# Kernel optimization log

Measured on AMD Instinct MI355X. Metric: run time of the kernel, lower is better.

## Reference

```python
import jax, jax.numpy as jnp
from jax import lax
import numpy as np

B, T, D_IN, H, L, D_OUT = 1024, 512, 6, 128, 3, 1


def _lstm_layer(xs, w_ih, w_hh, b_ih, b_hh):
    """xs: [B, T, Din]; w_ih: [4H, Din]; w_hh: [4H, H]. PyTorch gate order i,f,g,o."""
    Bq = xs.shape[0]
    Hq = w_hh.shape[1]
    # Precompute the input projection for all timesteps (compute-dense part).
    x_proj = jnp.einsum('btd,gd->btg', xs, w_ih) + (b_ih + b_hh)  # [B, T, 4H]

    def step(carry, xp):
        h, c = carry
        gates = xp + h @ w_hh.T  # [B, 4H]
        i, f, g, o = jnp.split(gates, 4, axis=-1)
        i = jax.nn.sigmoid(i)
        f = jax.nn.sigmoid(f)
        g = jnp.tanh(g)
        o = jax.nn.sigmoid(o)
        c = f * c + i * g
        h = o * jnp.tanh(c)
        return (h, c), h

    h0 = jnp.zeros((Bq, Hq), xs.dtype)
    c0 = jnp.zeros((Bq, Hq), xs.dtype)
    (_, _), hs = lax.scan(step, (h0, c0), jnp.swapaxes(x_proj, 0, 1))  # hs: [T, B, H]
    return jnp.swapaxes(hs, 0, 1)  # [B, T, H]


def setup_inputs() -> dict:
    key = jax.random.key(0)
    ks = jax.random.split(key, 16)
    s = 1.0 / np.sqrt(H)  # PyTorch LSTM init scale
    inp = {"x": jax.random.normal(ks[0], (B, T, D_IN), dtype=jnp.float32)}
    din = D_IN
    for l in range(L):
        inp[f"w_ih{l}"] = jax.random.uniform(ks[1 + 4 * l], (4 * H, din), minval=-s, maxval=s, dtype=jnp.float32)
        inp[f"w_hh{l}"] = jax.random.uniform(ks[2 + 4 * l], (4 * H, H), minval=-s, maxval=s, dtype=jnp.float32)
        inp[f"b_ih{l}"] = jax.random.uniform(ks[3 + 4 * l], (4 * H,), minval=-s, maxval=s, dtype=jnp.float32)
        inp[f"b_hh{l}"] = jax.random.uniform(ks[4 + 4 * l], (4 * H,), minval=-s, maxval=s, dtype=jnp.float32)
        din = H
    inp["fc_w"] = jax.random.uniform(ks[13], (D_OUT, H), minval=-s, maxval=s, dtype=jnp.float32)
    inp["fc_b"] = jax.random.uniform(ks[14], (D_OUT,), minval=-s, maxval=s, dtype=jnp.float32)
    return inp


def reference(x, w_ih0, w_hh0, b_ih0, b_hh0, w_ih1, w_hh1, b_ih1, b_hh1,
              w_ih2, w_hh2, b_ih2, b_hh2, fc_w, fc_b):
    # 3-layer LSTM (inference: dropout between layers is identity) + final Linear on last timestep.
    h = _lstm_layer(x, w_ih0, w_hh0, b_ih0, b_hh0)
    h = _lstm_layer(h, w_ih1, w_hh1, b_ih1, b_hh1)
    h = _lstm_layer(h, w_ih2, w_hh2, b_ih2, b_hh2)
    return h[:, -1, :] @ fc_w.T + fc_b  # [B, 1]
```

## Files before the change

kernel.cpp:

```cpp
#include <hip/hip_runtime.h>

#define TLEN  512
#define HID   128
#define RSLOT 16

typedef __attribute__((ext_vector_type(8))) short          bf16x8;
typedef __attribute__((ext_vector_type(4))) float          f32x4;
typedef __attribute__((ext_vector_type(2))) float          f32x2;
typedef __attribute__((ext_vector_type(4))) unsigned short u16x4;
typedef unsigned long long u64;

#define LOG2E  1.4426950408889634f
#define LOG2E2 2.8853900817779268f

template<bool B> struct BC { static constexpr bool value = B; };
template<int I>  struct IC { static constexpr int  value = I; };

__device__ __forceinline__ unsigned short f2bf(float f) {
    union { float f; unsigned u; } v; v.f = f;
    unsigned r = v.u + 0x7fffu + ((v.u >> 16) & 1u);
    return (unsigned short)(r >> 16);
}
__device__ __forceinline__ unsigned short f2bf_fast(float f) {
    union { float f; unsigned u; } v; v.f = f;
    return (unsigned short)((v.u + 0x8000u) >> 16);
}

__device__ __forceinline__ f32x2 exp2_2(f32x2 a) {
    f32x2 r; r.x = __builtin_exp2f(a.x); r.y = __builtin_exp2f(a.y); return r;
}
__device__ __forceinline__ f32x2 rcp_2(f32x2 a) {
    f32x2 r; r.x = __builtin_amdgcn_rcpf(a.x); r.y = __builtin_amdgcn_rcpf(a.y); return r;
}


__device__ __forceinline__ int flag_peek(const int* f) {
    return __hip_atomic_load(f, __ATOMIC_RELAXED, __HIP_MEMORY_SCOPE_AGENT);
}
__device__ __forceinline__ int flag_spin(const int* f, int v) {
    int x = flag_peek(f);
    while (x < v) { __builtin_amdgcn_s_sleep(1); x = flag_peek(f); }
    return x;
}
__device__ __forceinline__ void flag_pub(int* f, int v) {
    __hip_atomic_store(f, v, __ATOMIC_RELAXED, __HIP_MEMORY_SCOPE_WORKGROUP);
}

template<int MODE, bool CONS, bool PROD, bool WFC>
__device__ __forceinline__ void run_layer_p(
    const float* __restrict__ xin,
    const u64* __restrict__ rin, u64* __restrict__ rout,
    const int* pin_flag, int* cout_flag, const int* cin_flag, int* pout_flag,
    const float* __restrict__ wih, const float* __restrict__ whh,
    const float* __restrict__ bih, const float* __restrict__ bhh,
    unsigned short (* __restrict__ hbuf)[2048],
    unsigned short (* __restrict__ xbuf)[2048],
    float* __restrict__ fcred,
    const int tid, const int wave, const int lane,
    const int n16, const int quad, const int bbase)
{
    constexpr int NKTX = MODE ? 4 : 1;
    constexpr int DINL = MODE ? 128 : 6;

    bf16x8 Wfx[4][NKTX], Wfh[4][4];
    f32x4  bbv[4];
#pragma unroll
    for (int g = 0; g < 4; ++g) {
        const float sc = (g == 2) ? LOG2E2 : LOG2E;
        const int row = g * 128 + wave * 16 + n16;
        const float bg = (bih[row] + bhh[row]) * sc;
        f32x4 bi = {bg, bg, bg, bg};
        bbv[g] = bi;
#pragma unroll
        for (int kt = 0; kt < NKTX; ++kt) {
            bf16x8 wv;
#pragma unroll
            for (int j = 0; j < 8; ++j) {
                const int k = kt * 32 + quad * 8 + j;
                wv[j] = (short)f2bf(((k < DINL) ? wih[row * DINL + k] : 0.0f) * sc);
            }
            Wfx[g][kt] = wv;
        }
#pragma unroll
        for (int kt = 0; kt < 4; ++kt) {
            bf16x8 wv;
#pragma unroll
            for (int j = 0; j < 8; ++j) {
                const int k = kt * 32 + quad * 8 + j;
                wv[j] = (short)f2bf(whh[row * HID + k] * sc);
            }
            Wfh[g][kt] = wv;
        }
    }

    const int rof  = (lane ^ quad) * 8;
    const int j    = wave * 16 + n16;
    const int beta = ((j & 31) >> 3) & 3;
    const int wbase = ((j >> 5) * 64 + ((j & 31) >> 3) * 16 + quad * 4) * 8 + (j & 7);
    int wof[4];
#pragma unroll
    for (int r = 0; r < 4; ++r) wof[r] = wbase + ((r ^ beta) * 8);
    const int uof  = ((((tid >> 1) ^ ((tid >> 5) & 3))) << 3) + (tid & 1) * 4;
    const int xm = tid >> 5, xk = tid & 31;
    const int eiS = ((xk >> 3) * 16 + (xm ^ (xk >> 3))) * 8 + (xk & 7);

    { u16x4 z = {0, 0, 0, 0}; *(u16x4*)&hbuf[0][uof] = z; }
    u64 q0 = 0, q1 = 0, q2 = 0, qn = 0;
    float pfx0 = 0.0f;
    int pend = 0, cpend = 0;
    if constexpr (CONS) {
        flag_spin(pin_flag, 1);
        *(u64*)&xbuf[0][uof] =
            __hip_atomic_load(rin + tid, __ATOMIC_RELAXED, __HIP_MEMORY_SCOPE_AGENT);
        flag_spin(pin_flag, 2);
        *(u64*)&xbuf[1][uof] =
            __hip_atomic_load(rin + 512 + tid, __ATOMIC_RELAXED, __HIP_MEMORY_SCOPE_AGENT);
        pend = flag_spin(pin_flag, 5);
        q0 = __hip_atomic_load(rin + 2 * 512 + tid, __ATOMIC_RELAXED, __HIP_MEMORY_SCOPE_AGENT);
        q1 = __hip_atomic_load(rin + 3 * 512 + tid, __ATOMIC_RELAXED, __HIP_MEMORY_SCOPE_AGENT);
        q2 = __hip_atomic_load(rin + 4 * 512 + tid, __ATOMIC_RELAXED, __HIP_MEMORY_SCOPE_AGENT);
    } else {
        float v0 = (xk < DINL) ? xin[((bbase + xm) * TLEN + 0) * DINL + xk] : 0.0f;
        float v1 = (xk < DINL) ? xin[((bbase + xm) * TLEN + 1) * DINL + xk] : 0.0f;
        xbuf[0][eiS] = f2bf(v0);
        xbuf[1][eiS] = f2bf(v1);
        if (xk < DINL) pfx0 = xin[((bbase + xm) * TLEN + 2) * DINL + xk];
    }
    if constexpr (PROD) cpend = -(1 << 30);
    __syncthreads();

    f32x4 accA[4], accB[4];
#pragma unroll
    for (int kt = 0; kt < NKTX; ++kt) {
        bf16x8 a = *(const bf16x8*)&xbuf[0][rof + kt * 512];
#pragma unroll
        for (int g = 0; g < 4; ++g)
            accA[g] = __builtin_amdgcn_mfma_f32_16x16x32_bf16(
                a, Wfx[g][kt], (kt == 0) ? bbv[g] : accA[g], 0, 0, 0);
    }

    f32x2 cst2[2] = {{0.f, 0.f}, {0.f, 0.f}};
    float hf[4];

    auto step = [&](auto SHc, auto CMc, auto CURc, auto RDc, auto WRc,
                    f32x4 (&accC)[4], f32x4 (&accN)[4], int t) {
        constexpr bool SH  = decltype(SHc)::value;
        constexpr bool CM  = decltype(CMc)::value;
        constexpr int  CUR = decltype(CURc)::value;
        constexpr int  NXT = CUR ^ 1;
        constexpr int  RD  = decltype(RDc)::value;
        constexpr int  WR  = decltype(WRc)::value;
        __syncthreads();

        const unsigned short* __restrict__ hcur = hbuf[CUR];
        const unsigned short* __restrict__ xrd  = xbuf[RD];

        bf16x8 ha_[4], xa_[NKTX];
#pragma unroll
        for (int kt = 0; kt < 4; ++kt) ha_[kt] = *(const bf16x8*)&hcur[rof + kt * 512];
        if constexpr (SH) {
#pragma unroll
            for (int kt = 0; kt < NKTX; ++kt)
                xa_[kt] = *(const bf16x8*)&xrd[rof + kt * 512];
        }

        if constexpr (CONS) {
            if (t + 5 < TLEN) {
                if (pend < t + 6) pend = flag_spin(pin_flag, t + 6);
                qn = __hip_atomic_load(rin + ((t + 5) & (RSLOT - 1)) * 512 + tid,
                                       __ATOMIC_RELAXED, __HIP_MEMORY_SCOPE_AGENT);
                pend = flag_peek(pin_flag);
            }
        }
        if (tid == 0) {
            if constexpr (CONS) if ((t & 3) == 0) flag_pub(cout_flag, t + 5);
            if constexpr (PROD) if (t >= 2)       flag_pub(pout_flag, t - 1);
        }
        if constexpr (PROD) {
            if (t >= 1) {
                const int e = t - 1;
                if ((e & 3) == 0 && e + 4 > RSLOT && cpend < e + 4 - RSLOT)
                    cpend = flag_spin(cin_flag, e + 4 - RSLOT);
                u64 hv = *(const u64*)&hcur[uof];
                __hip_atomic_store(rout + (e & (RSLOT - 1)) * 512 + tid, hv,
                                   __ATOMIC_RELAXED, __HIP_MEMORY_SCOPE_WORKGROUP);
                if ((e & 3) == 1) cpend = flag_peek(cin_flag);
            }
        }
        float pfx1 = 0.0f;
        if constexpr (!CONS) {
            if (t + 3 < TLEN && xk < DINL)
                pfx1 = xin[((bbase + xm) * TLEN + (t + 3)) * DINL + xk];
        }

#pragma unroll
        for (int kt = 0; kt < 4; ++kt)
#pragma unroll
            for (int g = 0; g < 4; ++g)
                accC[g] = __builtin_amdgcn_mfma_f32_16x16x32_bf16(ha_[kt], Wfh[g][kt], accC[g], 0, 0, 0);

        if constexpr (SH) {
#pragma unroll
            for (int kt = 0; kt < NKTX; ++kt)
#pragma unroll
                for (int g = 0; g < 4; ++g)
                    accN[g] = __builtin_amdgcn_mfma_f32_16x16x32_bf16(
                        xa_[kt], Wfx[g][kt], (kt == 0) ? bbv[g] : accN[g], 0, 0, 0);
        }

        const f32x2 one = {1.0f, 1.0f};
#pragma unroll
        for (int p = 0; p < 2; ++p) {
            const f32x2 gi = {accC[0][2 * p], accC[0][2 * p + 1]};
            const f32x2 gf = {accC[1][2 * p], accC[1][2 * p + 1]};
            const f32x2 gg = {accC[2][2 * p], accC[2][2 * p + 1]};
            const f32x2 go = {accC[3][2 * p], accC[3][2 * p + 1]};
            const f32x2 A  = exp2_2(-gi);
            const f32x2 Fv = rcp_2(one + exp2_2(-gf));
            const f32x2 E  = exp2_2(-gg);
            const f32x2 D  = exp2_2(-go);
            const f32x2 ig = (one - E) * rcp_2((one + A) * (one + E));
            const f32x2 c  = Fv * cst2[p] + ig;
            cst2[p] = c;
            f32x2 y = c * (f32x2){LOG2E2, LOG2E2};
            y.x = fminf(fmaxf(y.x, -30.0f), 30.0f);
            y.y = fminf(fmaxf(y.y, -30.0f), 30.0f);
            const f32x2 Cn = exp2_2(-y);
            const f32x2 h2 = (one - Cn) * rcp_2((one + D) * (one + Cn));
            if constexpr (WFC) { hf[2 * p] = h2.x; hf[2 * p + 1] = h2.y; }
            hbuf[NXT][wof[2 * p]]     = f2bf_fast(h2.x);
            hbuf[NXT][wof[2 * p + 1]] = f2bf_fast(h2.y);
        }
        if constexpr (WFC) {
            if (t == TLEN - 1)
#pragma unroll
                for (int r = 0; r < 4; ++r)
                    fcred[(quad * 4 + r) * HID + wave * 16 + n16] = hf[r];
        }
        if constexpr (CM) {
            if constexpr (CONS) {
                *(u64*)&xbuf[WR][uof] = q0;
                q0 = q1; q1 = q2; q2 = qn;
            } else {
                xbuf[WR][eiS] = f2bf(pfx0);
                pfx0 = pfx1;
            }
        }
    };

    for (int t = 0; t < TLEN - 2; t += 6) {
        step(BC<true>{}, BC<true>{}, IC<0>{}, IC<1>{}, IC<2>{}, accA, accB, t);
        step(BC<true>{}, BC<true>{}, IC<1>{}, IC<2>{}, IC<0>{}, accB, accA, t + 1);
        step(BC<true>{}, BC<true>{}, IC<0>{}, IC<0>{}, IC<1>{}, accA, accB, t + 2);
        step(BC<true>{}, BC<true>{}, IC<1>{}, IC<1>{}, IC<2>{}, accB, accA, t + 3);
        step(BC<true>{}, BC<true>{}, IC<0>{}, IC<2>{}, IC<0>{}, accA, accB, t + 4);
        step(BC<true>{}, BC<true>{}, IC<1>{}, IC<0>{}, IC<1>{}, accB, accA, t + 5);
    }
    step(BC<true>{},  BC<false>{}, IC<0>{}, IC<1>{}, IC<2>{}, accA, accB, TLEN - 2);
    step(BC<false>{}, BC<false>{}, IC<1>{}, IC<2>{}, IC<0>{}, accB, accA, TLEN - 1);

    if constexpr (PROD) {
        __syncthreads();
        if (tid == 0) flag_pub(pout_flag, TLEN - 1);
        {
            flag_spin(cin_flag, TLEN - RSLOT);
            u64 hv = *(const u64*)&hbuf[TLEN & 1][uof];
            __hip_atomic_store(rout + ((TLEN - 1) & (RSLOT - 1)) * 512 + tid, hv,
                               __ATOMIC_RELAXED, __HIP_MEMORY_SCOPE_WORKGROUP);
        }
        __syncthreads();
        if (tid == 0) flag_pub(pout_flag, TLEN);
    }
}

extern "C" __global__ __launch_bounds__(512, 1)
void lstm3_pipe_kernel(const float* __restrict__ xin,
    const float* __restrict__ wih0, const float* __restrict__ whh0,
    const float* __restrict__ bih0, const float* __restrict__ bhh0,
    const float* __restrict__ wih1, const float* __restrict__ whh1,
    const float* __restrict__ bih1, const float* __restrict__ bhh1,
    const float* __restrict__ wih2, const float* __restrict__ whh2,
    const float* __restrict__ bih2, const float* __restrict__ bhh2,
    const float* __restrict__ fcw, const float* __restrict__ fcb,
    float* __restrict__ out,
    int* __restrict__ flags, u64* __restrict__ ring0, u64* __restrict__ ring1)
{
    __shared__ unsigned short hbuf[2][2048];
    __shared__ unsigned short xbuf[3][2048];
    __shared__ float fcred[16 * HID];

    const int tid   = threadIdx.x;
    const int wave  = tid >> 6;
    const int lane  = tid & 63;
    const int n16   = lane & 15;
    const int quad  = lane >> 4;

    const int xcd    = blockIdx.x & 7;
    const int grp    = blockIdx.x >> 3;
    const int layer  = grp % 3;
    const int sgroup = grp / 3;
    const int slice  = sgroup * 8 + xcd;
    const int bbase  = slice * 16;

    u64* r0 = ring0 + (size_t)slice * (RSLOT * 512);
    u64* r1 = ring1 + (size_t)slice * (RSLOT * 512);
    int* prod0 = flags + (size_t)(0 * 64 + slice) * 64;
    int* prod1 = flags + (size_t)(1 * 64 + slice) * 64;
    int* cons1 = flags + (size_t)(2 * 64 + slice) * 64;
    int* cons2 = flags + (size_t)(3 * 64 + slice) * 64;

    if (layer == 0) {
        run_layer_p<0, false, true, false>(xin, nullptr, r0,
            nullptr, nullptr, cons1, prod0,
            wih0, whh0, bih0, bhh0, hbuf, xbuf, fcred, tid, wave, lane, n16, quad, bbase);
    } else if (layer == 1) {
        run_layer_p<1, true, true, false>(nullptr, r0, r1,
            prod0, cons1, cons2, prod1,
            wih1, whh1, bih1, bhh1, hbuf, xbuf, fcred, tid, wave, lane, n16, quad, bbase);
    } else {
        run_layer_p<1, true, false, true>(nullptr, r1, nullptr,
            prod1, cons2, nullptr, nullptr,
            wih2, whh2, bih2, bhh2, hbuf, xbuf, fcred, tid, wave, lane, n16, quad, bbase);
        __syncthreads();
        if (tid < 16) {
            float s = 0.0f;
#pragma unroll 8
            for (int j = 0; j < HID; ++j) s += fcw[j] * fcred[tid * HID + j];
            out[bbase + tid] = s + fcb[0];
        }
    }
}

extern "C" void kernel_launch(void* const* d_in, const int* in_sizes, int n_in,
                              void* d_out, int out_size, void* d_ws, size_t ws_size,
                              hipStream_t stream) {
    (void)in_sizes; (void)n_in; (void)out_size; (void)ws_size;
    const float* x    = (const float*)d_in[0];
    const float* wih0 = (const float*)d_in[1];
    const float* whh0 = (const float*)d_in[2];
    const float* bih0 = (const float*)d_in[3];
    const float* bhh0 = (const float*)d_in[4];
    const float* wih1 = (const float*)d_in[5];
    const float* whh1 = (const float*)d_in[6];
    const float* bih1 = (const float*)d_in[7];
    const float* bhh1 = (const float*)d_in[8];
    const float* wih2 = (const float*)d_in[9];
    const float* whh2 = (const float*)d_in[10];
    const float* bih2 = (const float*)d_in[11];
    const float* bhh2 = (const float*)d_in[12];
    const float* fcw  = (const float*)d_in[13];
    const float* fcb  = (const float*)d_in[14];
    float* out = (float*)d_out;

    int* flags = (int*)d_ws;
    u64* ring0 = (u64*)((char*)d_ws + 65536);
    u64* ring1 = ring0 + (size_t)64 * RSLOT * 512;

    lstm3_pipe_kernel<<<dim3(192), dim3(512), 0, stream>>>(
        x, wih0, whh0, bih0, bhh0, wih1, whh1, bih1, bhh1,
        wih2, whh2, bih2, bhh2, fcw, fcb, out, flags, ring0, ring1);
}
```

Baseline: 766.2 us.

## Load consumer ring data directly into MFMA register fragments, bypassing LDS staging

Consumer layers now read the producer's ring buffer straight into per-lane bf16x8 MFMA A-fragments, using a 3-deep register ring indexed by the timestep. Previously each thread loaded one u64, staged it through an LDS x-buffer, and then reread it as fragments. The prefetch distance shrinks from 5 to 3 timesteps, and the credit flag published back to the producer changes to match. This removes the LDS writes and reads for the input projection, at the cost of more global atomic loads per lane, more registers held live, and less latency hiding.

```diff
diff --git a/kernel.cpp b/kernel.cpp
--- a/kernel.cpp
+++ b/kernel.cpp
@@ -104,21 +104,27 @@
     const int xm = tid >> 5, xk = tid & 31;
     const int eiS = ((xk >> 3) * 16 + (xm ^ (xk >> 3))) * 8 + (xk & 7);
 
+    bf16x8 xfr[3][4];
+    auto ring_frags = [&](int e, bf16x8 (&dst)[4]) {
+        const u64* pb = rin + (size_t)((e & (RSLOT - 1)) * 512 + 2 * lane);
+#pragma unroll
+        for (int kt = 0; kt < 4; ++kt) {
+            union { u64 d[2]; bf16x8 v; } u;
+            u.d[0] = __hip_atomic_load(pb + kt * 128,
+                                       __ATOMIC_RELAXED, __HIP_MEMORY_SCOPE_AGENT);
+            u.d[1] = __hip_atomic_load(pb + kt * 128 + 1,
+                                       __ATOMIC_RELAXED, __HIP_MEMORY_SCOPE_AGENT);
+            dst[kt] = u.v;
+        }
+    };
+
     { u16x4 z = {0, 0, 0, 0}; *(u16x4*)&hbuf[0][uof] = z; }
-    u64 q0 = 0, q1 = 0, q2 = 0, qn = 0;
     float pfx0 = 0.0f;
     int pend = 0, cpend = 0;
     if constexpr (CONS) {
-        flag_spin(pin_flag, 1);
-        *(u64*)&xbuf[0][uof] =
-            __hip_atomic_load(rin + tid, __ATOMIC_RELAXED, __HIP_MEMORY_SCOPE_AGENT);
-        flag_spin(pin_flag, 2);
-        *(u64*)&xbuf[1][uof] =
-            __hip_atomic_load(rin + 512 + tid, __ATOMIC_RELAXED, __HIP_MEMORY_SCOPE_AGENT);
-        pend = flag_spin(pin_flag, 5);
-        q0 = __hip_atomic_load(rin + 2 * 512 + tid, __ATOMIC_RELAXED, __HIP_MEMORY_SCOPE_AGENT);
-        q1 = __hip_atomic_load(rin + 3 * 512 + tid, __ATOMIC_RELAXED, __HIP_MEMORY_SCOPE_AGENT);
-        q2 = __hip_atomic_load(rin + 4 * 512 + tid, __ATOMIC_RELAXED, __HIP_MEMORY_SCOPE_AGENT);
+        flag_spin(pin_flag, 1); ring_frags(0, xfr[0]);
+        flag_spin(pin_flag, 2); ring_frags(1, xfr[1]);
+        pend = flag_spin(pin_flag, 3); ring_frags(2, xfr[2]);
     } else {
         float v0 = (xk < DINL) ? xin[((bbase + xm) * TLEN + 0) * DINL + xk] : 0.0f;
         float v1 = (xk < DINL) ? xin[((bbase + xm) * TLEN + 1) * DINL + xk] : 0.0f;
@@ -132,7 +138,9 @@
     f32x4 accA[4], accB[4];
 #pragma unroll
     for (int kt = 0; kt < NKTX; ++kt) {
-        bf16x8 a = *(const bf16x8*)&xbuf[0][rof + kt * 512];
+        bf16x8 a;
+        if constexpr (CONS) a = xfr[0][kt];
+        else                a = *(const bf16x8*)&xbuf[0][rof + kt * 512];
 #pragma unroll
         for (int g = 0; g < 4; ++g)
             accA[g] = __builtin_amdgcn_mfma_f32_16x16x32_bf16(
@@ -150,6 +158,7 @@
         constexpr int  NXT = CUR ^ 1;
         constexpr int  RD  = decltype(RDc)::value;
         constexpr int  WR  = decltype(WRc)::value;
+        constexpr int  LD  = (RD + 2) % 3;
         __syncthreads();
 
         const unsigned short* __restrict__ hcur = hbuf[CUR];
@@ -158,22 +167,21 @@
         bf16x8 ha_[4], xa_[NKTX];
 #pragma unroll
         for (int kt = 0; kt < 4; ++kt) ha_[kt] = *(const bf16x8*)&hcur[rof + kt * 512];
-        if constexpr (SH) {
+        if constexpr (SH && !CONS) {
 #pragma unroll
             for (int kt = 0; kt < NKTX; ++kt)
                 xa_[kt] = *(const bf16x8*)&xrd[rof + kt * 512];
         }
 
         if constexpr (CONS) {
-            if (t + 5 < TLEN) {
-                if (pend < t + 6) pend = flag_spin(pin_flag, t + 6);
-                qn = __hip_atomic_load(rin + ((t + 5) & (RSLOT - 1)) * 512 + tid,
-                                       __ATOMIC_RELAXED, __HIP_MEMORY_SCOPE_AGENT);
+            if (t + 3 < TLEN) {
+                if (pend < t + 4) pend = flag_spin(pin_flag, t + 4);
+                ring_frags(t + 3, xfr[LD]);
                 pend = flag_peek(pin_flag);
             }
         }
         if (tid == 0) {
-            if constexpr (CONS) if ((t & 3) == 0) flag_pub(cout_flag, t + 5);
+            if constexpr (CONS) if ((t & 3) == 0) flag_pub(cout_flag, t + 4);
             if constexpr (PROD) if (t >= 2)       flag_pub(pout_flag, t - 1);
         }
         if constexpr (PROD) {
@@ -201,11 +209,15 @@
 
         if constexpr (SH) {
 #pragma unroll
-            for (int kt = 0; kt < NKTX; ++kt)
+            for (int kt = 0; kt < NKTX; ++kt) {
+                bf16x8 a;
+                if constexpr (CONS) a = xfr[RD][kt];
+                else                a = xa_[kt];
 #pragma unroll
                 for (int g = 0; g < 4; ++g)
                     accN[g] = __builtin_amdgcn_mfma_f32_16x16x32_bf16(
-                        xa_[kt], Wfx[g][kt], (kt == 0) ? bbv[g] : accN[g], 0, 0, 0);
+                        a, Wfx[g][kt], (kt == 0) ? bbv[g] : accN[g], 0, 0, 0);
+            }
         }
 
         const f32x2 one = {1.0f, 1.0f};
@@ -237,14 +249,9 @@
                 for (int r = 0; r < 4; ++r)
                     fcred[(quad * 4 + r) * HID + wave * 16 + n16] = hf[r];
         }
-        if constexpr (CM) {
-            if constexpr (CONS) {
-                *(u64*)&xbuf[WR][uof] = q0;
-                q0 = q1; q1 = q2; q2 = qn;
-            } else {
-                xbuf[WR][eiS] = f2bf(pfx0);
-                pfx0 = pfx1;
-            }
+        if constexpr (CM && !CONS) {
+            xbuf[WR][eiS] = f2bf(pfx0);
+            pfx0 = pfx1;
         }
     };
 
```

New measurement: 884.2 us. 1.15x slower.
